# Optimization experiments

Measured on AMD Instinct MI355X. Metric: run time of the kernel, lower is better.

Reference implementation:

```python
import jax, jax.numpy as jnp
import numpy as np

N_NODES = 100000
N_EDGES = 1600000
IN_DIM = 128
HID = 32
HEADS = 4
OUT_DIM = 40
NEG_SLOPE = 0.2
BN_EPS = 1e-5


def setup_inputs() -> dict:
    key = jax.random.key(0)
    ks = jax.random.split(key, 13)
    x = jax.random.normal(ks[0], (N_NODES, IN_DIM), jnp.float32)
    edge_index = jax.random.randint(ks[1], (2, N_EDGES), 0, N_NODES, dtype=jnp.int32)
    s0 = 1.0 / np.sqrt(IN_DIM)
    s1 = 1.0 / np.sqrt(HEADS * HID)
    return {
        "x": x,
        "edge_index": edge_index,
        # layer 0: GATConv(IN_DIM -> HID, HEADS heads, concat)
        "W0": jax.random.normal(ks[2], (IN_DIM, HEADS * HID), jnp.float32) * s0,
        "a_src0": jax.random.normal(ks[3], (HEADS, HID), jnp.float32) * s0,
        "a_dst0": jax.random.normal(ks[4], (HEADS, HID), jnp.float32) * s0,
        "b0": jnp.zeros((HEADS * HID,), jnp.float32),
        # BatchNorm1d(HEADS*HID)
        "gamma0": jnp.ones((HEADS * HID,), jnp.float32),
        "beta0": jnp.zeros((HEADS * HID,), jnp.float32),
        # layer 1: GATConv(HEADS*HID -> OUT_DIM, 1 head, mean)
        "W1": jax.random.normal(ks[5], (HEADS * HID, OUT_DIM), jnp.float32) * s1,
        "a_src1": jax.random.normal(ks[6], (1, OUT_DIM), jnp.float32) * s1,
        "a_dst1": jax.random.normal(ks[7], (1, OUT_DIM), jnp.float32) * s1,
        "b1": jnp.zeros((OUT_DIM,), jnp.float32),
    }


def gat_conv(x, src, dst, n_nodes, W, a_src, a_dst, b, heads, concat):
    # linear transform: [N, H, C]
    h = (x @ W).reshape(n_nodes, heads, -1)
    # per-node attention logits [N, H]
    alpha_src = (h * a_src).sum(-1)
    alpha_dst = (h * a_dst).sum(-1)
    # per-edge raw attention [E, H]
    e = jax.nn.leaky_relu(alpha_src[src] + alpha_dst[dst], NEG_SLOPE)
    # softmax over incoming edges of each destination node
    m = jax.ops.segment_max(e, dst, num_segments=n_nodes)  # self-loops -> no empty segment
    ex = jnp.exp(e - m[dst])
    den = jax.ops.segment_sum(ex, dst, num_segments=n_nodes)
    # weighted scatter-aggregate of messages [E, H, C] -> [N, H, C]
    out = jax.ops.segment_sum(ex[:, :, None] * h[src], dst, num_segments=n_nodes)
    out = out / den[:, :, None]
    out = out.reshape(n_nodes, -1) if concat else out.mean(axis=1)
    return out + b


def batch_norm(x, gamma, beta):
    mu = x.mean(axis=0)
    var = x.var(axis=0)
    return (x - mu) * jax.lax.rsqrt(var + BN_EPS) * gamma + beta


def reference(x, edge_index, W0, a_src0, a_dst0, b0, gamma0, beta0,
              W1, a_src1, a_dst1, b1):
    n = x.shape[0]
    loop = jnp.arange(n, dtype=edge_index.dtype)
    src = jnp.concatenate([edge_index[0], loop])  # add self-loops (PyG default)
    dst = jnp.concatenate([edge_index[1], loop])
    # layer 0: GATConv -> BN -> ELU (dropout p=0 / eval -> identity)
    h = gat_conv(x, src, dst, n, W0, a_src0, a_dst0, b0, HEADS, True)
    h = jax.nn.elu(batch_norm(h, gamma0, beta0))
    # layer 1: GATConv, 1 head, mean aggregation, no BN/act
    out = gat_conv(h, src, dst, n, W1, a_src1, a_dst1, b1, 1, False)
    return out
```

## Files before the change

kernel.cpp:

```cpp
#include <hip/hip_runtime.h>
#include <hip/hip_bf16.h>
#include <math.h>

#define NN   100000
#define EE   1600000
#define ETOT (NN + EE)
#define IND  128
#define HD   128
#define OD   40
#define NEG  0.2f
#define BNEPS 1e-5f

typedef __attribute__((ext_vector_type(8))) short bf16x8;
typedef __attribute__((ext_vector_type(4))) float f32x4;

__device__ __forceinline__ float lrelu(float x) { return x > 0.f ? x : NEG * x; }

__device__ __forceinline__ unsigned pack_bf16(float a, float b) {
  unsigned ua = __float_as_uint(a), ub = __float_as_uint(b);
  ua = (ua + 0x7fffu + ((ua >> 16) & 1u)) >> 16;
  ub = (ub + 0x7fffu + ((ub >> 16) & 1u)) >> 16;
  return ua | (ub << 16);
}
__device__ __forceinline__ float bf16_lo(unsigned v) { return __uint_as_float(v << 16); }
__device__ __forceinline__ float bf16_hi(unsigned v) { return __uint_as_float(v & 0xffff0000u); }

__global__ __launch_bounds__(256) void w0pack_kernel(const float* __restrict__ W0,
                                                     unsigned* __restrict__ w0t) {
  int idx = blockIdx.x * 256 + threadIdx.x;
  if (idx >= 128 * 64) return;
  int n = idx & 127, kp = idx >> 7;
  float lo = W0[(size_t)(2 * kp) * 128 + n];
  float hi = W0[(size_t)(2 * kp + 1) * 128 + n];
  w0t[n * 64 + kp] = pack_bf16(lo, hi);
}

__global__ __launch_bounds__(256) void gemm0_kernel(const float* __restrict__ x,
                                                    const unsigned* __restrict__ w0t,
                                                    const float* __restrict__ a_src0,
                                                    const float* __restrict__ a_dst0,
                                                    unsigned* __restrict__ h0b,
                                                    float* __restrict__ asrc0,
                                                    float* __restrict__ adst0) {
  __shared__ __align__(16) unsigned As[64][68];
  __shared__ __align__(16) unsigned Wt[128][68];
  int t = threadIdx.x;
  int rowbase = blockIdx.x * 64;
  for (int idx = t; idx < 128 * 64; idx += 256) {
    Wt[idx >> 6][idx & 63] = w0t[idx];
  }
  for (int idx = t; idx < 64 * 64; idx += 256) {
    int row = idx >> 6, kp = idx & 63;
    int r = rowbase + row;
    int rc = r < NN ? r : NN - 1;
    float2 v = *(const float2*)&x[(size_t)rc * 128 + kp * 2];
    As[row][kp] = pack_bf16(v.x, v.y);
  }
  __syncthreads();

  int lane = t & 63, w = t >> 6;
  int mrow = lane & 15, g = lane >> 4;
  f32x4 acc[8];
#pragma unroll
  for (int nt = 0; nt < 8; nt++) acc[nt] = (f32x4){0.f, 0.f, 0.f, 0.f};
#pragma unroll
  for (int ks = 0; ks < 4; ks++) {
    bf16x8 a = *(const bf16x8*)&As[w * 16 + mrow][ks * 16 + g * 4];
#pragma unroll
    for (int nt = 0; nt < 8; nt++) {
      bf16x8 b = *(const bf16x8*)&Wt[nt * 16 + mrow][ks * 16 + g * 4];
      acc[nt] = __builtin_amdgcn_mfma_f32_16x16x32_bf16(a, b, acc[nt], 0, 0, 0);
    }
  }
  int col = lane & 15;
  float as_[8], ad_[8];
#pragma unroll
  for (int nt = 0; nt < 8; nt++) {
    as_[nt] = a_src0[nt * 16 + col];
    ad_[nt] = a_dst0[nt * 16 + col];
  }
#pragma unroll
  for (int reg = 0; reg < 4; reg++) {
    int r = rowbase + w * 16 + g * 4 + reg;
    bool rok = r < NN;
    float hs0 = acc[0][reg] * as_[0] + acc[1][reg] * as_[1];
    float hs1 = acc[2][reg] * as_[2] + acc[3][reg] * as_[3];
    float hs2 = acc[4][reg] * as_[4] + acc[5][reg] * as_[5];
    float hs3 = acc[6][reg] * as_[6] + acc[7][reg] * as_[7];
    float hd0 = acc[0][reg] * ad_[0] + acc[1][reg] * ad_[1];
    float hd1 = acc[2][reg] * ad_[2] + acc[3][reg] * ad_[3];
    float hd2 = acc[4][reg] * ad_[4] + acc[5][reg] * ad_[5];
    float hd3 = acc[6][reg] * ad_[6] + acc[7][reg] * ad_[7];
#pragma unroll
    for (int mk = 1; mk < 16; mk <<= 1) {
      hs0 += __shfl_xor(hs0, mk); hs1 += __shfl_xor(hs1, mk);
      hs2 += __shfl_xor(hs2, mk); hs3 += __shfl_xor(hs3, mk);
      hd0 += __shfl_xor(hd0, mk); hd1 += __shfl_xor(hd1, mk);
      hd2 += __shfl_xor(hd2, mk); hd3 += __shfl_xor(hd3, mk);
    }
    if ((lane & 15) == 0 && rok) {
      asrc0[r * 4 + 0] = hs0; asrc0[r * 4 + 1] = hs1;
      asrc0[r * 4 + 2] = hs2; asrc0[r * 4 + 3] = hs3;
      adst0[r * 4 + 0] = hd0; adst0[r * 4 + 1] = hd1;
      adst0[r * 4 + 2] = hd2; adst0[r * 4 + 3] = hd3;
    }
#pragma unroll
    for (int nt = 0; nt < 8; nt++) {
      float v = acc[nt][reg];
      float nv = __shfl_xor(v, 1);
      if (!(col & 1) && rok) h0b[(size_t)r * 64 + nt * 8 + (col >> 1)] = pack_bf16(v, nv);
    }
  }
}

__global__ void degrank_kernel(const int* __restrict__ ei, int* __restrict__ deg,
                               int* __restrict__ rank) {
  int i4 = (blockIdx.x * blockDim.x + threadIdx.x) * 4;
  if (i4 >= ETOT) return;
  int4 d;
  if (i4 < EE) d = *(const int4*)&ei[EE + i4];
  else         d = make_int4(i4 - EE, i4 - EE + 1, i4 - EE + 2, i4 - EE + 3);
  int4 r;
  r.x = atomicAdd(&deg[d.x], 1);
  r.y = atomicAdd(&deg[d.y], 1);
  r.z = atomicAdd(&deg[d.z], 1);
  r.w = atomicAdd(&deg[d.w], 1);
  *(int4*)&rank[i4] = r;
}

__global__ __launch_bounds__(256) void scanA_kernel(const int* __restrict__ deg,
                                                    int* __restrict__ scanned,
                                                    int* __restrict__ blocksums) {
  __shared__ int s[256];
  int t = threadIdx.x;
  int i = blockIdx.x * 256 + t;
  int v = (i < NN) ? deg[i] : 0;
  s[t] = v;
  __syncthreads();
  for (int off = 1; off < 256; off <<= 1) {
    int add = (t >= off) ? s[t - off] : 0;
    __syncthreads();
    s[t] += add;
    __syncthreads();
  }
  if (i < NN) scanned[i] = s[t];
  if (t == 255) blocksums[blockIdx.x] = s[255];
}

__global__ __launch_bounds__(512) void scanB_kernel(int* __restrict__ blocksums, int NB) {
  __shared__ int s[512];
  int t = threadIdx.x;
  int v = (t < NB) ? blocksums[t] : 0;
  s[t] = v;
  __syncthreads();
  for (int off = 1; off < 512; off <<= 1) {
    int add = (t >= off) ? s[t - off] : 0;
    __syncthreads();
    s[t] += add;
    __syncthreads();
  }
  if (t < NB) blocksums[t] = s[t] - v;
}

__global__ __launch_bounds__(256) void scanC_kernel(const int* __restrict__ scanned,
                                                    const int* __restrict__ deg,
                                                    const int* __restrict__ blocksums,
                                                    int* __restrict__ rowptr) {
  int i = blockIdx.x * 256 + threadIdx.x;
  if (i < NN) rowptr[i] = blocksums[blockIdx.x] + scanned[i] - deg[i];
  if (i == 0) rowptr[NN] = ETOT;
}

__global__ void scatter_kernel(const int* __restrict__ ei, const int* __restrict__ rowptr,
                               const int* __restrict__ rank, int* __restrict__ csr_src) {
  int i4 = (blockIdx.x * blockDim.x + threadIdx.x) * 4;
  if (i4 >= ETOT) return;
  int4 s, d;
  if (i4 < EE) {
    s = *(const int4*)&ei[i4];
    d = *(const int4*)&ei[EE + i4];
  } else {
    s = make_int4(i4 - EE, i4 - EE + 1, i4 - EE + 2, i4 - EE + 3);
    d = s;
  }
  int4 rk = *(const int4*)&rank[i4];
  int p0 = rowptr[d.x] + rk.x;
  int p1 = rowptr[d.y] + rk.y;
  int p2 = rowptr[d.z] + rk.z;
  int p3 = rowptr[d.w] + rk.w;
  csr_src[p0] = s.x;
  csr_src[p1] = s.y;
  csr_src[p2] = s.z;
  csr_src[p3] = s.w;
}

__global__ __launch_bounds__(256) void agg0_kernel(const int* __restrict__ csr_src,
                                                   const int* __restrict__ rowptr,
                                                   const float* __restrict__ asrc0,
                                                   const float* __restrict__ adst0,
                                                   const unsigned* __restrict__ h0b,
                                                   const float* __restrict__ b0,
                                                   unsigned* __restrict__ agg0b) {
  __shared__ float ws[16][4][17];
  __shared__ int   ss[16][16];
  int t = threadIdx.x;
  int grp = t >> 4;
  int p   = t & 15;
  int n = blockIdx.x * 16 + grp;
  if (n >= NN) return;
  int start = rowptr[n], end = rowptr[n + 1];
  float4 ad = *(const float4*)&adst0[(size_t)n * 4];
  int head = p >> 2;
  float a0 = 0.f, a1 = 0.f, a2 = 0.f, a3 = 0.f, a4 = 0.f, a5 = 0.f, a6 = 0.f, a7 = 0.f;
  float d0 = 0.f, d1 = 0.f, d2 = 0.f, d3 = 0.f;

  for (int base = start; base < end; base += 16) {
    int cnt = min(16, end - base);
    if (p < cnt) {
      int s = csr_src[base + p];
      float4 as = *(const float4*)&asrc0[(size_t)s * 4];
      float w0 = __expf(lrelu(as.x + ad.x));
      float w1 = __expf(lrelu(as.y + ad.y));
      float w2 = __expf(lrelu(as.z + ad.z));
      float w3 = __expf(lrelu(as.w + ad.w));
      d0 += w0; d1 += w1; d2 += w2; d3 += w3;
      ss[grp][p] = s;
      ws[grp][0][p] = w0;
      ws[grp][1][p] = w1;
      ws[grp][2][p] = w2;
      ws[grp][3][p] = w3;
    }
    __builtin_amdgcn_wave_barrier();
    if (cnt == 16) {
      uint4 hv[16];
#pragma unroll
      for (int e = 0; e < 16; e++) {
        int s = ss[grp][e];
        hv[e] = *(const uint4*)&h0b[(size_t)s * 64 + p * 4];
      }
#pragma unroll
      for (int e = 0; e < 16; e++) {
        float w = ws[grp][head][e];
        a0 += w * bf16_lo(hv[e].x); a1 += w * bf16_hi(hv[e].x);
        a2 += w * bf16_lo(hv[e].y); a3 += w * bf16_hi(hv[e].y);
        a4 += w * bf16_lo(hv[e].z); a5 += w * bf16_hi(hv[e].z);
        a6 += w * bf16_lo(hv[e].w); a7 += w * bf16_hi(hv[e].w);
      }
    } else {
      for (int eb = 0; eb < cnt; eb += 4) {
        int e0 = eb, e1 = eb + 1, e2 = eb + 2, e3 = eb + 3;
        float w0 = ws[grp][head][e0];
        float w1 = (e1 < cnt) ? ws[grp][head][e1] : 0.f;
        float w2 = (e2 < cnt) ? ws[grp][head][e2] : 0.f;
        float w3 = (e3 < cnt) ? ws[grp][head][e3] : 0.f;
        int s0 = ss[grp][e0];
        int s1 = ss[grp][(e1 < cnt) ? e1 : e0];
        int s2 = ss[grp][(e2 < cnt) ? e2 : e0];
        int s3 = ss[grp][(e3 < cnt) ? e3 : e0];
        uint4 h0v = *(const uint4*)&h0b[(size_t)s0 * 64 + p * 4];
        uint4 h1v = *(const uint4*)&h0b[(size_t)s1 * 64 + p * 4];
        uint4 h2v = *(const uint4*)&h0b[(size_t)s2 * 64 + p * 4];
        uint4 h3v = *(const uint4*)&h0b[(size_t)s3 * 64 + p * 4];
        a0 += w0 * bf16_lo(h0v.x); a1 += w0 * bf16_hi(h0v.x);
        a2 += w0 * bf16_lo(h0v.y); a3 += w0 * bf16_hi(h0v.y);
        a4 += w0 * bf16_lo(h0v.z); a5 += w0 * bf16_hi(h0v.z);
        a6 += w0 * bf16_lo(h0v.w); a7 += w0 * bf16_hi(h0v.w);
        a0 += w1 * bf16_lo(h1v.x); a1 += w1 * bf16_hi(h1v.x);
        a2 += w1 * bf16_lo(h1v.y); a3 += w1 * bf16_hi(h1v.y);
        a4 += w1 * bf16_lo(h1v.z); a5 += w1 * bf16_hi(h1v.z);
        a6 += w1 * bf16_lo(h1v.w); a7 += w1 * bf16_hi(h1v.w);
        a0 += w2 * bf16_lo(h2v.x); a1 += w2 * bf16_hi(h2v.x);
        a2 += w2 * bf16_lo(h2v.y); a3 += w2 * bf16_hi(h2v.y);
        a4 += w2 * bf16_lo(h2v.z); a5 += w2 * bf16_hi(h2v.z);
        a6 += w2 * bf16_lo(h2v.w); a7 += w2 * bf16_hi(h2v.w);
        a0 += w3 * bf16_lo(h3v.x); a1 += w3 * bf16_hi(h3v.x);
        a2 += w3 * bf16_lo(h3v.y); a3 += w3 * bf16_hi(h3v.y);
        a4 += w3 * bf16_lo(h3v.z); a5 += w3 * bf16_hi(h3v.z);
        a6 += w3 * bf16_lo(h3v.w); a7 += w3 * bf16_hi(h3v.w);
      }
    }
    __builtin_amdgcn_wave_barrier();
  }
#pragma unroll
  for (int mk = 1; mk < 16; mk <<= 1) {
    d0 += __shfl_xor(d0, mk);
    d1 += __shfl_xor(d1, mk);
    d2 += __shfl_xor(d2, mk);
    d3 += __shfl_xor(d3, mk);
  }
  float dh = head == 0 ? d0 : head == 1 ? d1 : head == 2 ? d2 : d3;
  float rd = 1.f / dh;
  int c = p * 8;
  float4 b1v = *(const float4*)&b0[c];
  float4 b2v = *(const float4*)&b0[c + 4];
  float o0 = a0 * rd + b1v.x, o1 = a1 * rd + b1v.y;
  float o2 = a2 * rd + b1v.z, o3 = a3 * rd + b1v.w;
  float o4 = a4 * rd + b2v.x, o5 = a5 * rd + b2v.y;
  float o6 = a6 * rd + b2v.z, o7 = a7 * rd + b2v.w;
  uint4 o;
  o.x = pack_bf16(o0, o1);
  o.y = pack_bf16(o2, o3);
  o.z = pack_bf16(o4, o5);
  o.w = pack_bf16(o6, o7);
  *(uint4*)&agg0b[(size_t)n * 64 + p * 4] = o;
}

__global__ __launch_bounds__(256) void bnstats_kernel(const unsigned* __restrict__ agg0b,
                                                      float* __restrict__ bnsum,
                                                      float* __restrict__ bnsq) {
  int t = threadIdx.x;
  int c2 = t & 63;
  int rg = t >> 6;
  float sl = 0.f, sh = 0.f, ql = 0.f, qh = 0.f;
  for (int r = blockIdx.x * 4 + rg; r < NN; r += 2048) {
    unsigned u = agg0b[(size_t)r * 64 + c2];
    float lo = bf16_lo(u), hi = bf16_hi(u);
    sl += lo; sh += hi;
    ql += lo * lo; qh += hi * hi;
  }
  __shared__ float L1[256], L2[256], L3[256], L4[256];
  L1[t] = sl; L2[t] = sh; L3[t] = ql; L4[t] = qh;
  __syncthreads();
  if (t < 64) {
    sl = L1[t] + L1[t + 64] + L1[t + 128] + L1[t + 192];
    sh = L2[t] + L2[t + 64] + L2[t + 128] + L2[t + 192];
    ql = L3[t] + L3[t + 64] + L3[t + 128] + L3[t + 192];
    qh = L4[t] + L4[t + 64] + L4[t + 128] + L4[t + 192];
    atomicAdd(&bnsum[2 * t], sl);
    atomicAdd(&bnsum[2 * t + 1], sh);
    atomicAdd(&bnsq[2 * t], ql);
    atomicAdd(&bnsq[2 * t + 1], qh);
  }
}

__global__ void bnfinal_kernel(const float* __restrict__ bnsum, const float* __restrict__ bnsq,
                               const float* __restrict__ gamma, const float* __restrict__ beta,
                               float* __restrict__ bnscale, float* __restrict__ bnshift) {
  int c = threadIdx.x;
  float mu = bnsum[c] / (float)NN;
  float var = bnsq[c] / (float)NN - mu * mu;
  float sc = gamma[c] / sqrtf(var + BNEPS);
  bnscale[c] = sc;
  bnshift[c] = beta[c] - mu * sc;
}

__global__ __launch_bounds__(256) void gemm1_kernel(const unsigned* __restrict__ agg0b,
                                                    const float* __restrict__ bnscale,
                                                    const float* __restrict__ bnshift,
                                                    const float* __restrict__ W1,
                                                    const float* __restrict__ a_src1,
                                                    const float* __restrict__ a_dst1,
                                                    unsigned* __restrict__ h1b,
                                                    float* __restrict__ asrc1,
                                                    float* __restrict__ adst1) {
  __shared__ __align__(16) unsigned As[64][68];
  __shared__ __align__(16) unsigned Wt[48][68];
  int t = threadIdx.x;
  int rowbase = blockIdx.x * 64;

  for (int idx = t; idx < 48 * 64; idx += 256) {
    int c = idx >> 6, kp = idx & 63;
    float lo = (c < OD) ? W1[(size_t)(2 * kp) * OD + c] : 0.f;
    float hi = (c < OD) ? W1[(size_t)(2 * kp + 1) * OD + c] : 0.f;
    Wt[c][kp] = pack_bf16(lo, hi);
  }
  for (int idx = t; idx < 64 * 16; idx += 256) {
    int row = idx >> 4, c4 = idx & 15;
    int r = rowbase + row;
    int rc = r < NN ? r : NN - 1;
    int k = c4 * 8;
    uint4 hv = *(const uint4*)&agg0b[(size_t)rc * 64 + c4 * 4];
    float4 sc1 = *(const float4*)&bnscale[k];
    float4 sc2 = *(const float4*)&bnscale[k + 4];
    float4 sh1 = *(const float4*)&bnshift[k];
    float4 sh2 = *(const float4*)&bnshift[k + 4];
    float y0 = bf16_lo(hv.x) * sc1.x + sh1.x;
    float y1 = bf16_hi(hv.x) * sc1.y + sh1.y;
    float y2 = bf16_lo(hv.y) * sc1.z + sh1.z;
    float y3 = bf16_hi(hv.y) * sc1.w + sh1.w;
    float y4 = bf16_lo(hv.z) * sc2.x + sh2.x;
    float y5 = bf16_hi(hv.z) * sc2.y + sh2.y;
    float y6 = bf16_lo(hv.w) * sc2.z + sh2.z;
    float y7 = bf16_hi(hv.w) * sc2.w + sh2.w;
    y0 = y0 > 0.f ? y0 : expm1f(y0);
    y1 = y1 > 0.f ? y1 : expm1f(y1);
    y2 = y2 > 0.f ? y2 : expm1f(y2);
    y3 = y3 > 0.f ? y3 : expm1f(y3);
    y4 = y4 > 0.f ? y4 : expm1f(y4);
    y5 = y5 > 0.f ? y5 : expm1f(y5);
    y6 = y6 > 0.f ? y6 : expm1f(y6);
    y7 = y7 > 0.f ? y7 : expm1f(y7);
    As[row][c4 * 4 + 0] = pack_bf16(y0, y1);
    As[row][c4 * 4 + 1] = pack_bf16(y2, y3);
    As[row][c4 * 4 + 2] = pack_bf16(y4, y5);
    As[row][c4 * 4 + 3] = pack_bf16(y6, y7);
  }
  __syncthreads();

  int lane = t & 63, w = t >> 6;
  int mrow = lane & 15, g = lane >> 4;
  f32x4 acc0 = {0.f, 0.f, 0.f, 0.f};
  f32x4 acc1 = {0.f, 0.f, 0.f, 0.f};
  f32x4 acc2 = {0.f, 0.f, 0.f, 0.f};
#pragma unroll
  for (int ks = 0; ks < 4; ks++) {
    bf16x8 a = *(const bf16x8*)&As[w * 16 + mrow][ks * 16 + g * 4];
    bf16x8 b0v = *(const bf16x8*)&Wt[mrow][ks * 16 + g * 4];
    bf16x8 b1v = *(const bf16x8*)&Wt[16 + mrow][ks * 16 + g * 4];
    bf16x8 b2v = *(const bf16x8*)&Wt[32 + mrow][ks * 16 + g * 4];
    acc0 = __builtin_amdgcn_mfma_f32_16x16x32_bf16(a, b0v, acc0, 0, 0, 0);
    acc1 = __builtin_amdgcn_mfma_f32_16x16x32_bf16(a, b1v, acc1, 0, 0, 0);
    acc2 = __builtin_amdgcn_mfma_f32_16x16x32_bf16(a, b2v, acc2, 0, 0, 0);
  }
  int col = lane & 15;
  float as0 = (col < OD)      ? a_src1[col]      : 0.f;
  float as1 = (16 + col < OD) ? a_src1[16 + col] : 0.f;
  float as2 = (32 + col < OD) ? a_src1[32 + col] : 0.f;
  float ad0 = (col < OD)      ? a_dst1[col]      : 0.f;
  float ad1 = (16 + col < OD) ? a_dst1[16 + col] : 0.f;
  float ad2 = (32 + col < OD) ? a_dst1[32 + col] : 0.f;
#pragma unroll
  for (int reg = 0; reg < 4; reg++) {
    int r = rowbase + w * 16 + g * 4 + reg;
    float v0 = acc0[reg], v1 = acc1[reg], v2 = acc2[reg];
    float ps = v0 * as0 + v1 * as1 + v2 * as2;
    float pd = v0 * ad0 + v1 * ad1 + v2 * ad2;
#pragma unroll
    for (int mk = 1; mk < 16; mk <<= 1) { ps += __shfl_xor(ps, mk); pd += __shfl_xor(pd, mk); }
    bool rok = r < NN;
    if ((lane & 15) == 0 && rok) { asrc1[r] = ps; adst1[r] = pd; }
    float n0 = __shfl_xor(v0, 1), n1 = __shfl_xor(v1, 1), n2 = __shfl_xor(v2, 1);
    if (!(col & 1) && rok) {
      h1b[(size_t)r * 20 + ((col) >> 1)]      = pack_bf16(v0, n0);
      h1b[(size_t)r * 20 + ((16 + col) >> 1)] = pack_bf16(v1, n1);
      if (32 + col < OD) h1b[(size_t)r * 20 + ((32 + col) >> 1)] = pack_bf16(v2, n2);
    }
  }
}

__global__ __launch_bounds__(256) void agg1_kernel(const int* __restrict__ csr_src,
                                                   const int* __restrict__ rowptr,
                                                   const float* __restrict__ asrc1,
                                                   const float* __restrict__ adst1,
                                                   const unsigned* __restrict__ h1b,
                                                   const float* __restrict__ b1,
                                                   float* __restrict__ out) {
  __shared__ float ws[4][64];
  __shared__ int   ss[4][64];
  int t = threadIdx.x;
  int lane = t & 63, wv = t >> 6;
  int n = blockIdx.x * 4 + wv;
  if (n >= NN) return;
  int start = rowptr[n], end = rowptr[n + 1];
  float ad = adst1[n];
  int esub = lane / 20;
  int chan = lane - esub * 20;
  float dsum = 0.f, acc0 = 0.f, acc1 = 0.f;
  for (int base = start; base < end; base += 64) {
    int cnt = min(64, end - base);
    if (lane < cnt) {
      int s = csr_src[base + lane];
      float w = __expf(lrelu(asrc1[s] + ad));
      dsum += w;
      ss[wv][lane] = s;
      ws[wv][lane] = w;
    }
    __builtin_amdgcn_wave_barrier();
    if (lane < 60) {
      int e = esub;
      for (; e + 9 < cnt; e += 12) {
        int s0 = ss[wv][e], s1 = ss[wv][e + 3], s2 = ss[wv][e + 6], s3 = ss[wv][e + 9];
        unsigned u0 = h1b[(size_t)s0 * 20 + chan];
        unsigned u1 = h1b[(size_t)s1 * 20 + chan];
        unsigned u2 = h1b[(size_t)s2 * 20 + chan];
        unsigned u3 = h1b[(size_t)s3 * 20 + chan];
        float w0 = ws[wv][e], w1 = ws[wv][e + 3], w2 = ws[wv][e + 6], w3 = ws[wv][e + 9];
        acc0 += w0 * bf16_lo(u0); acc1 += w0 * bf16_hi(u0);
        acc0 += w1 * bf16_lo(u1); acc1 += w1 * bf16_hi(u1);
        acc0 += w2 * bf16_lo(u2); acc1 += w2 * bf16_hi(u2);
        acc0 += w3 * bf16_lo(u3); acc1 += w3 * bf16_hi(u3);
      }
      for (; e < cnt; e += 3) {
        int s = ss[wv][e];
        float w = ws[wv][e];
        unsigned hv = h1b[(size_t)s * 20 + chan];
        acc0 += w * bf16_lo(hv);
        acc1 += w * bf16_hi(hv);
      }
    }
    __builtin_amdgcn_wave_barrier();
  }
#pragma unroll
  for (int mk = 1; mk < 64; mk <<= 1) dsum += __shfl_xor(dsum, mk);
  float rd = 1.f / dsum;
  float b0v = __shfl(acc0, lane + 20);
  float c0v = __shfl(acc0, lane + 40);
  float b1v = __shfl(acc1, lane + 20);
  float c1v = __shfl(acc1, lane + 40);
  if (lane < 20) {
    float2 o;
    o.x = (acc0 + b0v + c0v) * rd + b1[lane * 2];
    o.y = (acc1 + b1v + c1v) * rd + b1[lane * 2 + 1];
    *(float2*)&out[(size_t)n * 40 + lane * 2] = o;
  }
}

extern "C" void kernel_launch(void* const* d_in, const int* in_sizes, int n_in,
                              void* d_out, int out_size, void* d_ws, size_t ws_size,
                              hipStream_t stream) {
  const float* x       = (const float*)d_in[0];
  const int*   ei      = (const int*)d_in[1];
  const float* W0      = (const float*)d_in[2];
  const float* a_src0  = (const float*)d_in[3];
  const float* a_dst0  = (const float*)d_in[4];
  const float* b0      = (const float*)d_in[5];
  const float* gamma0  = (const float*)d_in[6];
  const float* beta0   = (const float*)d_in[7];
  const float* W1      = (const float*)d_in[8];
  const float* a_src1  = (const float*)d_in[9];
  const float* a_dst1  = (const float*)d_in[10];
  const float* b1      = (const float*)d_in[11];
  float* out = (float*)d_out;

  char* ws = (char*)d_ws;
  size_t off = 0;
  auto alloc = [&](size_t bytes) {
    void* p = ws + off;
    off += (bytes + 255) & ~(size_t)255;
    return p;
  };
  int*   deg      = (int*)alloc((size_t)NN * 4);
  float* bnsum    = (float*)alloc(128 * 4);
  float* bnsq     = (float*)alloc(128 * 4);
  unsigned* h0b   = (unsigned*)alloc((size_t)NN * 64 * 4);
  unsigned* agg0b = (unsigned*)alloc((size_t)NN * 64 * 4);
  unsigned* h1b   = (unsigned*)alloc((size_t)NN * 20 * 4);
  float* asrc0    = (float*)alloc((size_t)NN * 4 * 4);
  float* adst0    = (float*)alloc((size_t)NN * 4 * 4);
  float* asrc1    = (float*)alloc((size_t)NN * 4);
  float* adst1    = (float*)alloc((size_t)NN * 4);
  float* bnscale  = (float*)alloc(128 * 4);
  float* bnshift  = (float*)alloc(128 * 4);
  int*   rowptr   = (int*)alloc((size_t)(NN + 1) * 4);
  int*   scanned  = (int*)alloc((size_t)NN * 4);
  int*   csr      = (int*)alloc((size_t)ETOT * 4);
  int*   rank     = (int*)alloc((size_t)ETOT * 4);
  int*   bsums    = (int*)alloc(512 * 4);
  unsigned* w0t   = (unsigned*)alloc(128 * 64 * 4);
  (void)ws_size; (void)in_sizes; (void)n_in; (void)out_size;

  size_t zbytes = (char*)(bnsq + 128) - (char*)deg;
  hipMemsetAsync(deg, 0, zbytes, stream);

  const int NB = (NN + 255) / 256;
  const int e4grid = (ETOT / 4 + 255) / 256;

  w0pack_kernel<<<32, 256, 0, stream>>>(W0, w0t);
  gemm0_kernel<<<(NN + 63) / 64, 256, 0, stream>>>(x, w0t, a_src0, a_dst0, h0b, asrc0, adst0);
  degrank_kernel<<<e4grid, 256, 0, stream>>>(ei, deg, rank);
  scanA_kernel<<<NB, 256, 0, stream>>>(deg, scanned, bsums);
  scanB_kernel<<<1, 512, 0, stream>>>(bsums, NB);
  scanC_kernel<<<NB, 256, 0, stream>>>(scanned, deg, bsums, rowptr);
  scatter_kernel<<<e4grid, 256, 0, stream>>>(ei, rowptr, rank, csr);
  agg0_kernel<<<(NN + 15) / 16, 256, 0, stream>>>(csr, rowptr, asrc0, adst0, h0b, b0, agg0b);
  bnstats_kernel<<<512, 256, 0, stream>>>(agg0b, bnsum, bnsq);
  bnfinal_kernel<<<1, 128, 0, stream>>>(bnsum, bnsq, gamma0, beta0, bnscale, bnshift);
  gemm1_kernel<<<(NN + 63) / 64, 256, 0, stream>>>(agg0b, bnscale, bnshift, W1, a_src1, a_dst1,
                                                   h1b, asrc1, adst1);
  agg1_kernel<<<(NN + 3) / 4, 256, 0, stream>>>(csr, rowptr, asrc1, adst1, h1b, b1, out);
}
```

Before: 333.1 us.

## Fuse BN statistics into aggregation, merge prep kernels, widen agg1 loads

Folds W0 packing into the degree/rank kernel, computes BatchNorm sum and sum-of-squares inside agg0 using wave shuffles and bucketed atomics, and finalizes BN scale/shift at the top of gemm1. This removes the separate bnstats and bnfinal launches and the extra pass over agg0b. It also drops agg0's specialized 16-edge unrolled path and changes agg1 to 8-byte loads with 4 channels per lane. Fusing the stats adds atomic contention, which is spread over 16 buckets, and the agg0 grid now assumes NN is divisible by 16.

```diff
diff --git a/kernel.cpp b/kernel.cpp
--- a/kernel.cpp
+++ b/kernel.cpp
@@ -10,6 +10,7 @@
 #define OD   40
 #define NEG  0.2f
 #define BNEPS 1e-5f
+#define NBKT 16
 
 typedef __attribute__((ext_vector_type(8))) short bf16x8;
 typedef __attribute__((ext_vector_type(4))) float f32x4;
@@ -25,14 +26,27 @@
 __device__ __forceinline__ float bf16_lo(unsigned v) { return __uint_as_float(v << 16); }
 __device__ __forceinline__ float bf16_hi(unsigned v) { return __uint_as_float(v & 0xffff0000u); }
 
-__global__ __launch_bounds__(256) void w0pack_kernel(const float* __restrict__ W0,
-                                                     unsigned* __restrict__ w0t) {
-  int idx = blockIdx.x * 256 + threadIdx.x;
-  if (idx >= 128 * 64) return;
-  int n = idx & 127, kp = idx >> 7;
-  float lo = W0[(size_t)(2 * kp) * 128 + n];
-  float hi = W0[(size_t)(2 * kp + 1) * 128 + n];
-  w0t[n * 64 + kp] = pack_bf16(lo, hi);
+__global__ void prep_kernel(const float* __restrict__ W0, unsigned* __restrict__ w0t,
+                            const int* __restrict__ ei, int* __restrict__ deg,
+                            int* __restrict__ rank) {
+  int gid = blockIdx.x * blockDim.x + threadIdx.x;
+  if (gid < 128 * 64) {
+    int n = gid & 127, kp = gid >> 7;
+    float lo = W0[(size_t)(2 * kp) * 128 + n];
+    float hi = W0[(size_t)(2 * kp + 1) * 128 + n];
+    w0t[n * 64 + kp] = pack_bf16(lo, hi);
+  }
+  int i4 = gid * 4;
+  if (i4 >= ETOT) return;
+  int4 d;
+  if (i4 < EE) d = *(const int4*)&ei[EE + i4];
+  else         d = make_int4(i4 - EE, i4 - EE + 1, i4 - EE + 2, i4 - EE + 3);
+  int4 r;
+  r.x = atomicAdd(&deg[d.x], 1);
+  r.y = atomicAdd(&deg[d.y], 1);
+  r.z = atomicAdd(&deg[d.z], 1);
+  r.w = atomicAdd(&deg[d.w], 1);
+  *(int4*)&rank[i4] = r;
 }
 
 __global__ __launch_bounds__(256) void gemm0_kernel(const float* __restrict__ x,
@@ -111,21 +125,6 @@
       if (!(col & 1) && rok) h0b[(size_t)r * 64 + nt * 8 + (col >> 1)] = pack_bf16(v, nv);
     }
   }
-}
-
-__global__ void degrank_kernel(const int* __restrict__ ei, int* __restrict__ deg,
-                               int* __restrict__ rank) {
-  int i4 = (blockIdx.x * blockDim.x + threadIdx.x) * 4;
-  if (i4 >= ETOT) return;
-  int4 d;
-  if (i4 < EE) d = *(const int4*)&ei[EE + i4];
-  else         d = make_int4(i4 - EE, i4 - EE + 1, i4 - EE + 2, i4 - EE + 3);
-  int4 r;
-  r.x = atomicAdd(&deg[d.x], 1);
-  r.y = atomicAdd(&deg[d.y], 1);
-  r.z = atomicAdd(&deg[d.z], 1);
-  r.w = atomicAdd(&deg[d.w], 1);
-  *(int4*)&rank[i4] = r;
 }
 
 __global__ __launch_bounds__(256) void scanA_kernel(const int* __restrict__ deg,
@@ -200,14 +199,16 @@
                                                    const float* __restrict__ adst0,
                                                    const unsigned* __restrict__ h0b,
                                                    const float* __restrict__ b0,
-                                                   unsigned* __restrict__ agg0b) {
+                                                   unsigned* __restrict__ agg0b,
+                                                   float* __restrict__ bnsumB,
+                                                   float* __restrict__ bnsqB) {
   __shared__ float ws[16][4][17];
   __shared__ int   ss[16][16];
+  __shared__ float Lsum[4][16][8], Lsq[4][16][8];
   int t = threadIdx.x;
   int grp = t >> 4;
   int p   = t & 15;
   int n = blockIdx.x * 16 + grp;
-  if (n >= NN) return;
   int start = rowptr[n], end = rowptr[n + 1];
   float4 ad = *(const float4*)&adst0[(size_t)n * 4];
   int head = p >> 2;
@@ -231,53 +232,36 @@
       ws[grp][3][p] = w3;
     }
     __builtin_amdgcn_wave_barrier();
-    if (cnt == 16) {
-      uint4 hv[16];
-#pragma unroll
-      for (int e = 0; e < 16; e++) {
-        int s = ss[grp][e];
-        hv[e] = *(const uint4*)&h0b[(size_t)s * 64 + p * 4];
-      }
-#pragma unroll
-      for (int e = 0; e < 16; e++) {
-        float w = ws[grp][head][e];
-        a0 += w * bf16_lo(hv[e].x); a1 += w * bf16_hi(hv[e].x);
-        a2 += w * bf16_lo(hv[e].y); a3 += w * bf16_hi(hv[e].y);
-        a4 += w * bf16_lo(hv[e].z); a5 += w * bf16_hi(hv[e].z);
-        a6 += w * bf16_lo(hv[e].w); a7 += w * bf16_hi(hv[e].w);
-      }
-    } else {
-      for (int eb = 0; eb < cnt; eb += 4) {
-        int e0 = eb, e1 = eb + 1, e2 = eb + 2, e3 = eb + 3;
-        float w0 = ws[grp][head][e0];
-        float w1 = (e1 < cnt) ? ws[grp][head][e1] : 0.f;
-        float w2 = (e2 < cnt) ? ws[grp][head][e2] : 0.f;
-        float w3 = (e3 < cnt) ? ws[grp][head][e3] : 0.f;
-        int s0 = ss[grp][e0];
-        int s1 = ss[grp][(e1 < cnt) ? e1 : e0];
-        int s2 = ss[grp][(e2 < cnt) ? e2 : e0];
-        int s3 = ss[grp][(e3 < cnt) ? e3 : e0];
-        uint4 h0v = *(const uint4*)&h0b[(size_t)s0 * 64 + p * 4];
-        uint4 h1v = *(const uint4*)&h0b[(size_t)s1 * 64 + p * 4];
-        uint4 h2v = *(const uint4*)&h0b[(size_t)s2 * 64 + p * 4];
-        uint4 h3v = *(const uint4*)&h0b[(size_t)s3 * 64 + p * 4];
-        a0 += w0 * bf16_lo(h0v.x); a1 += w0 * bf16_hi(h0v.x);
-        a2 += w0 * bf16_lo(h0v.y); a3 += w0 * bf16_hi(h0v.y);
-        a4 += w0 * bf16_lo(h0v.z); a5 += w0 * bf16_hi(h0v.z);
-        a6 += w0 * bf16_lo(h0v.w); a7 += w0 * bf16_hi(h0v.w);
-        a0 += w1 * bf16_lo(h1v.x); a1 += w1 * bf16_hi(h1v.x);
-        a2 += w1 * bf16_lo(h1v.y); a3 += w1 * bf16_hi(h1v.y);
-        a4 += w1 * bf16_lo(h1v.z); a5 += w1 * bf16_hi(h1v.z);
-        a6 += w1 * bf16_lo(h1v.w); a7 += w1 * bf16_hi(h1v.w);
-        a0 += w2 * bf16_lo(h2v.x); a1 += w2 * bf16_hi(h2v.x);
-        a2 += w2 * bf16_lo(h2v.y); a3 += w2 * bf16_hi(h2v.y);
-        a4 += w2 * bf16_lo(h2v.z); a5 += w2 * bf16_hi(h2v.z);
-        a6 += w2 * bf16_lo(h2v.w); a7 += w2 * bf16_hi(h2v.w);
-        a0 += w3 * bf16_lo(h3v.x); a1 += w3 * bf16_hi(h3v.x);
-        a2 += w3 * bf16_lo(h3v.y); a3 += w3 * bf16_hi(h3v.y);
-        a4 += w3 * bf16_lo(h3v.z); a5 += w3 * bf16_hi(h3v.z);
-        a6 += w3 * bf16_lo(h3v.w); a7 += w3 * bf16_hi(h3v.w);
-      }
+    for (int eb = 0; eb < cnt; eb += 4) {
+      int e0 = eb, e1 = eb + 1, e2 = eb + 2, e3 = eb + 3;
+      float w0 = ws[grp][head][e0];
+      float w1 = (e1 < cnt) ? ws[grp][head][e1] : 0.f;
+      float w2 = (e2 < cnt) ? ws[grp][head][e2] : 0.f;
+      float w3 = (e3 < cnt) ? ws[grp][head][e3] : 0.f;
+      int s0 = ss[grp][e0];
+      int s1 = ss[grp][(e1 < cnt) ? e1 : e0];
+      int s2 = ss[grp][(e2 < cnt) ? e2 : e0];
+      int s3 = ss[grp][(e3 < cnt) ? e3 : e0];
+      uint4 h0v = *(const uint4*)&h0b[(size_t)s0 * 64 + p * 4];
+      uint4 h1v = *(const uint4*)&h0b[(size_t)s1 * 64 + p * 4];
+      uint4 h2v = *(const uint4*)&h0b[(size_t)s2 * 64 + p * 4];
+      uint4 h3v = *(const uint4*)&h0b[(size_t)s3 * 64 + p * 4];
+      a0 += w0 * bf16_lo(h0v.x); a1 += w0 * bf16_hi(h0v.x);
+      a2 += w0 * bf16_lo(h0v.y); a3 += w0 * bf16_hi(h0v.y);
+      a4 += w0 * bf16_lo(h0v.z); a5 += w0 * bf16_hi(h0v.z);
+      a6 += w0 * bf16_lo(h0v.w); a7 += w0 * bf16_hi(h0v.w);
+      a0 += w1 * bf16_lo(h1v.x); a1 += w1 * bf16_hi(h1v.x);
+      a2 += w1 * bf16_lo(h1v.y); a3 += w1 * bf16_hi(h1v.y);
+      a4 += w1 * bf16_lo(h1v.z); a5 += w1 * bf16_hi(h1v.z);
+      a6 += w1 * bf16_lo(h1v.w); a7 += w1 * bf16_hi(h1v.w);
+      a0 += w2 * bf16_lo(h2v.x); a1 += w2 * bf16_hi(h2v.x);
+      a2 += w2 * bf16_lo(h2v.y); a3 += w2 * bf16_hi(h2v.y);
+      a4 += w2 * bf16_lo(h2v.z); a5 += w2 * bf16_hi(h2v.z);
+      a6 += w2 * bf16_lo(h2v.w); a7 += w2 * bf16_hi(h2v.w);
+      a0 += w3 * bf16_lo(h3v.x); a1 += w3 * bf16_hi(h3v.x);
+      a2 += w3 * bf16_lo(h3v.y); a3 += w3 * bf16_hi(h3v.y);
+      a4 += w3 * bf16_lo(h3v.z); a5 += w3 * bf16_hi(h3v.z);
+      a6 += w3 * bf16_lo(h3v.w); a7 += w3 * bf16_hi(h3v.w);
     }
     __builtin_amdgcn_wave_barrier();
   }
@@ -303,50 +287,48 @@
   o.z = pack_bf16(o4, o5);
   o.w = pack_bf16(o6, o7);
   *(uint4*)&agg0b[(size_t)n * 64 + p * 4] = o;
-}
-
-__global__ __launch_bounds__(256) void bnstats_kernel(const unsigned* __restrict__ agg0b,
-                                                      float* __restrict__ bnsum,
-                                                      float* __restrict__ bnsq) {
-  int t = threadIdx.x;
-  int c2 = t & 63;
-  int rg = t >> 6;
-  float sl = 0.f, sh = 0.f, ql = 0.f, qh = 0.f;
-  for (int r = blockIdx.x * 4 + rg; r < NN; r += 2048) {
-    unsigned u = agg0b[(size_t)r * 64 + c2];
-    float lo = bf16_lo(u), hi = bf16_hi(u);
-    sl += lo; sh += hi;
-    ql += lo * lo; qh += hi * hi;
-  }
-  __shared__ float L1[256], L2[256], L3[256], L4[256];
-  L1[t] = sl; L2[t] = sh; L3[t] = ql; L4[t] = qh;
+
+  float s0 = o0, s1 = o1, s2 = o2, s3 = o3, s4 = o4, s5 = o5, s6 = o6, s7 = o7;
+  float q0 = o0 * o0, q1 = o1 * o1, q2 = o2 * o2, q3 = o3 * o3;
+  float q4 = o4 * o4, q5 = o5 * o5, q6 = o6 * o6, q7 = o7 * o7;
+#pragma unroll
+  for (int mk = 16; mk < 64; mk <<= 1) {
+    s0 += __shfl_xor(s0, mk); s1 += __shfl_xor(s1, mk);
+    s2 += __shfl_xor(s2, mk); s3 += __shfl_xor(s3, mk);
+    s4 += __shfl_xor(s4, mk); s5 += __shfl_xor(s5, mk);
+    s6 += __shfl_xor(s6, mk); s7 += __shfl_xor(s7, mk);
+    q0 += __shfl_xor(q0, mk); q1 += __shfl_xor(q1, mk);
+    q2 += __shfl_xor(q2, mk); q3 += __shfl_xor(q3, mk);
+    q4 += __shfl_xor(q4, mk); q5 += __shfl_xor(q5, mk);
+    q6 += __shfl_xor(q6, mk); q7 += __shfl_xor(q7, mk);
+  }
+  int lane = t & 63, wv = t >> 6;
+  if (lane < 16) {
+    Lsum[wv][lane][0] = s0; Lsum[wv][lane][1] = s1;
+    Lsum[wv][lane][2] = s2; Lsum[wv][lane][3] = s3;
+    Lsum[wv][lane][4] = s4; Lsum[wv][lane][5] = s5;
+    Lsum[wv][lane][6] = s6; Lsum[wv][lane][7] = s7;
+    Lsq[wv][lane][0] = q0; Lsq[wv][lane][1] = q1;
+    Lsq[wv][lane][2] = q2; Lsq[wv][lane][3] = q3;
+    Lsq[wv][lane][4] = q4; Lsq[wv][lane][5] = q5;
+    Lsq[wv][lane][6] = q6; Lsq[wv][lane][7] = q7;
+  }
   __syncthreads();
-  if (t < 64) {
-    sl = L1[t] + L1[t + 64] + L1[t + 128] + L1[t + 192];
-    sh = L2[t] + L2[t + 64] + L2[t + 128] + L2[t + 192];
-    ql = L3[t] + L3[t + 64] + L3[t + 128] + L3[t + 192];
-    qh = L4[t] + L4[t + 64] + L4[t + 128] + L4[t + 192];
-    atomicAdd(&bnsum[2 * t], sl);
-    atomicAdd(&bnsum[2 * t + 1], sh);
-    atomicAdd(&bnsq[2 * t], ql);
-    atomicAdd(&bnsq[2 * t + 1], qh);
-  }
-}
-
-__global__ void bnfinal_kernel(const float* __restrict__ bnsum, const float* __restrict__ bnsq,
-                               const float* __restrict__ gamma, const float* __restrict__ beta,
-                               float* __restrict__ bnscale, float* __restrict__ bnshift) {
-  int c = threadIdx.x;
-  float mu = bnsum[c] / (float)NN;
-  float var = bnsq[c] / (float)NN - mu * mu;
-  float sc = gamma[c] / sqrtf(var + BNEPS);
-  bnscale[c] = sc;
-  bnshift[c] = beta[c] - mu * sc;
+  if (t < 128) {
+    int pp = t >> 3, jj = t & 7;
+    float s = Lsum[0][pp][jj] + Lsum[1][pp][jj] + Lsum[2][pp][jj] + Lsum[3][pp][jj];
+    float q = Lsq[0][pp][jj] + Lsq[1][pp][jj] + Lsq[2][pp][jj] + Lsq[3][pp][jj];
+    int bkt = blockIdx.x & (NBKT - 1);
+    atomicAdd(&bnsumB[bkt * 128 + t], s);
+    atomicAdd(&bnsqB[bkt * 128 + t], q);
+  }
 }
 
 __global__ __launch_bounds__(256) void gemm1_kernel(const unsigned* __restrict__ agg0b,
-                                                    const float* __restrict__ bnscale,
-                                                    const float* __restrict__ bnshift,
+                                                    const float* __restrict__ bnsumB,
+                                                    const float* __restrict__ bnsqB,
+                                                    const float* __restrict__ gamma,
+                                                    const float* __restrict__ beta,
                                                     const float* __restrict__ W1,
                                                     const float* __restrict__ a_src1,
                                                     const float* __restrict__ a_dst1,
@@ -355,33 +337,44 @@
                                                     float* __restrict__ adst1) {
   __shared__ __align__(16) unsigned As[64][68];
   __shared__ __align__(16) unsigned Wt[48][68];
+  __shared__ float bnsc[128], bnsh[128];
   int t = threadIdx.x;
   int rowbase = blockIdx.x * 64;
 
+  if (t < 128) {
+    float s = 0.f, q = 0.f;
+#pragma unroll
+    for (int k = 0; k < NBKT; k++) {
+      s += bnsumB[k * 128 + t];
+      q += bnsqB[k * 128 + t];
+    }
+    float mu = s / (float)NN;
+    float var = q / (float)NN - mu * mu;
+    float sc = gamma[t] / sqrtf(var + BNEPS);
+    bnsc[t] = sc;
+    bnsh[t] = beta[t] - mu * sc;
+  }
   for (int idx = t; idx < 48 * 64; idx += 256) {
     int c = idx >> 6, kp = idx & 63;
     float lo = (c < OD) ? W1[(size_t)(2 * kp) * OD + c] : 0.f;
     float hi = (c < OD) ? W1[(size_t)(2 * kp + 1) * OD + c] : 0.f;
     Wt[c][kp] = pack_bf16(lo, hi);
   }
+  __syncthreads();
   for (int idx = t; idx < 64 * 16; idx += 256) {
     int row = idx >> 4, c4 = idx & 15;
     int r = rowbase + row;
     int rc = r < NN ? r : NN - 1;
     int k = c4 * 8;
     uint4 hv = *(const uint4*)&agg0b[(size_t)rc * 64 + c4 * 4];
-    float4 sc1 = *(const float4*)&bnscale[k];
-    float4 sc2 = *(const float4*)&bnscale[k + 4];
-    float4 sh1 = *(const float4*)&bnshift[k];
-    float4 sh2 = *(const float4*)&bnshift[k + 4];
-    float y0 = bf16_lo(hv.x) * sc1.x + sh1.x;
-    float y1 = bf16_hi(hv.x) * sc1.y + sh1.y;
-    float y2 = bf16_lo(hv.y) * sc1.z + sh1.z;
-    float y3 = bf16_hi(hv.y) * sc1.w + sh1.w;
-    float y4 = bf16_lo(hv.z) * sc2.x + sh2.x;
-    float y5 = bf16_hi(hv.z) * sc2.y + sh2.y;
-    float y6 = bf16_lo(hv.w) * sc2.z + sh2.z;
-    float y7 = bf16_hi(hv.w) * sc2.w + sh2.w;
+    float y0 = bf16_lo(hv.x) * bnsc[k + 0] + bnsh[k + 0];
+    float y1 = bf16_hi(hv.x) * bnsc[k + 1] + bnsh[k + 1];
+    float y2 = bf16_lo(hv.y) * bnsc[k + 2] + bnsh[k + 2];
+    float y3 = bf16_hi(hv.y) * bnsc[k + 3] + bnsh[k + 3];
+    float y4 = bf16_lo(hv.z) * bnsc[k + 4] + bnsh[k + 4];
+    float y5 = bf16_hi(hv.z) * bnsc[k + 5] + bnsh[k + 5];
+    float y6 = bf16_lo(hv.w) * bnsc[k + 6] + bnsh[k + 6];
+    float y7 = bf16_hi(hv.w) * bnsc[k + 7] + bnsh[k + 7];
     y0 = y0 > 0.f ? y0 : expm1f(y0);
     y1 = y1 > 0.f ? y1 : expm1f(y1);
     y2 = y2 > 0.f ? y2 : expm1f(y2);
@@ -453,9 +446,10 @@
   if (n >= NN) return;
   int start = rowptr[n], end = rowptr[n + 1];
   float ad = adst1[n];
-  int esub = lane / 20;
-  int chan = lane - esub * 20;
-  float dsum = 0.f, acc0 = 0.f, acc1 = 0.f;
+  int esub = lane / 10;
+  int c2   = lane - esub * 10;
+  float dsum = 0.f;
+  float acc0 = 0.f, acc1 = 0.f, acc2 = 0.f, acc3 = 0.f;
   for (int base = start; base < end; base += 64) {
     int cnt = min(64, end - base);
     if (lane < cnt) {
@@ -468,24 +462,28 @@
     __builtin_amdgcn_wave_barrier();
     if (lane < 60) {
       int e = esub;
-      for (; e + 9 < cnt; e += 12) {
-        int s0 = ss[wv][e], s1 = ss[wv][e + 3], s2 = ss[wv][e + 6], s3 = ss[wv][e + 9];
-        unsigned u0 = h1b[(size_t)s0 * 20 + chan];
-        unsigned u1 = h1b[(size_t)s1 * 20 + chan];
-        unsigned u2 = h1b[(size_t)s2 * 20 + chan];
-        unsigned u3 = h1b[(size_t)s3 * 20 + chan];
-        float w0 = ws[wv][e], w1 = ws[wv][e + 3], w2 = ws[wv][e + 6], w3 = ws[wv][e + 9];
-        acc0 += w0 * bf16_lo(u0); acc1 += w0 * bf16_hi(u0);
-        acc0 += w1 * bf16_lo(u1); acc1 += w1 * bf16_hi(u1);
-        acc0 += w2 * bf16_lo(u2); acc1 += w2 * bf16_hi(u2);
-        acc0 += w3 * bf16_lo(u3); acc1 += w3 * bf16_hi(u3);
+      for (; e + 18 < cnt; e += 24) {
+        int s0 = ss[wv][e], s1 = ss[wv][e + 6], s2 = ss[wv][e + 12], s3 = ss[wv][e + 18];
+        uint2 u0 = *(const uint2*)&h1b[(size_t)s0 * 20 + c2 * 2];
+        uint2 u1 = *(const uint2*)&h1b[(size_t)s1 * 20 + c2 * 2];
+        uint2 u2 = *(const uint2*)&h1b[(size_t)s2 * 20 + c2 * 2];
+        uint2 u3 = *(const uint2*)&h1b[(size_t)s3 * 20 + c2 * 2];
+        float w0 = ws[wv][e], w1 = ws[wv][e + 6], w2 = ws[wv][e + 12], w3 = ws[wv][e + 18];
+        acc0 += w0 * bf16_lo(u0.x); acc1 += w0 * bf16_hi(u0.x);
+        acc2 += w0 * bf16_lo(u0.y); acc3 += w0 * bf16_hi(u0.y);
+        acc0 += w1 * bf16_lo(u1.x); acc1 += w1 * bf16_hi(u1.x);
+        acc2 += w1 * bf16_lo(u1.y); acc3 += w1 * bf16_hi(u1.y);
+        acc0 += w2 * bf16_lo(u2.x); acc1 += w2 * bf16_hi(u2.x);
+        acc2 += w2 * bf16_lo(u2.y); acc3 += w2 * bf16_hi(u2.y);
+        acc0 += w3 * bf16_lo(u3.x); acc1 += w3 * bf16_hi(u3.x);
+        acc2 += w3 * bf16_lo(u3.y); acc3 += w3 * bf16_hi(u3.y);
       }
-      for (; e < cnt; e += 3) {
+      for (; e < cnt; e += 6) {
         int s = ss[wv][e];
         float w = ws[wv][e];
-        unsigned hv = h1b[(size_t)s * 20 + chan];
-        acc0 += w * bf16_lo(hv);
-        acc1 += w * bf16_hi(hv);
+        uint2 u = *(const uint2*)&h1b[(size_t)s * 20 + c2 * 2];
+        acc0 += w * bf16_lo(u.x); acc1 += w * bf16_hi(u.x);
+        acc2 += w * bf16_lo(u.y); acc3 += w * bf16_hi(u.y);
       }
     }
     __builtin_amdgcn_wave_barrier();
@@ -493,15 +491,30 @@
 #pragma unroll
   for (int mk = 1; mk < 64; mk <<= 1) dsum += __shfl_xor(dsum, mk);
   float rd = 1.f / dsum;
-  float b0v = __shfl(acc0, lane + 20);
-  float c0v = __shfl(acc0, lane + 40);
-  float b1v = __shfl(acc1, lane + 20);
-  float c1v = __shfl(acc1, lane + 40);
-  if (lane < 20) {
-    float2 o;
-    o.x = (acc0 + b0v + c0v) * rd + b1[lane * 2];
-    o.y = (acc1 + b1v + c1v) * rd + b1[lane * 2 + 1];
-    *(float2*)&out[(size_t)n * 40 + lane * 2] = o;
+  float p01 = __shfl(acc0, lane + 10), p02 = __shfl(acc0, lane + 20);
+  float p03 = __shfl(acc0, lane + 30), p04 = __shfl(acc0, lane + 40);
+  float p05 = __shfl(acc0, lane + 50);
+  float p11 = __shfl(acc1, lane + 10), p12 = __shfl(acc1, lane + 20);
+  float p13 = __shfl(acc1, lane + 30), p14 = __shfl(acc1, lane + 40);
+  float p15 = __shfl(acc1, lane + 50);
+  float p21 = __shfl(acc2, lane + 10), p22 = __shfl(acc2, lane + 20);
+  float p23 = __shfl(acc2, lane + 30), p24 = __shfl(acc2, lane + 40);
+  float p25 = __shfl(acc2, lane + 50);
+  float p31 = __shfl(acc3, lane + 10), p32 = __shfl(acc3, lane + 20);
+  float p33 = __shfl(acc3, lane + 30), p34 = __shfl(acc3, lane + 40);
+  float p35 = __shfl(acc3, lane + 50);
+  if (lane < 10) {
+    float t0 = acc0 + p01 + p02 + p03 + p04 + p05;
+    float t1 = acc1 + p11 + p12 + p13 + p14 + p15;
+    float t2 = acc2 + p21 + p22 + p23 + p24 + p25;
+    float t3 = acc3 + p31 + p32 + p33 + p34 + p35;
+    float4 bv = *(const float4*)&b1[lane * 4];
+    float4 o;
+    o.x = t0 * rd + bv.x;
+    o.y = t1 * rd + bv.y;
+    o.z = t2 * rd + bv.z;
+    o.w = t3 * rd + bv.w;
+    *(float4*)&out[(size_t)n * 40 + lane * 4] = o;
   }
 }
 
@@ -530,8 +543,8 @@
     return p;
   };
   int*   deg      = (int*)alloc((size_t)NN * 4);
-  float* bnsum    = (float*)alloc(128 * 4);
-  float* bnsq     = (float*)alloc(128 * 4);
+  float* bnsumB   = (float*)alloc(NBKT * 128 * 4);
+  float* bnsqB    = (float*)alloc(NBKT * 128 * 4);
   unsigned* h0b   = (unsigned*)alloc((size_t)NN * 64 * 4);
   unsigned* agg0b = (unsigned*)alloc((size_t)NN * 64 * 4);
   unsigned* h1b   = (unsigned*)alloc((size_t)NN * 20 * 4);
@@ -539,8 +552,6 @@
   float* adst0    = (float*)alloc((size_t)NN * 4 * 4);
   float* asrc1    = (float*)alloc((size_t)NN * 4);
   float* adst1    = (float*)alloc((size_t)NN * 4);
-  float* bnscale  = (float*)alloc(128 * 4);
-  float* bnshift  = (float*)alloc(128 * 4);
   int*   rowptr   = (int*)alloc((size_t)(NN + 1) * 4);
   int*   scanned  = (int*)alloc((size_t)NN * 4);
   int*   csr      = (int*)alloc((size_t)ETOT * 4);
@@ -549,23 +560,21 @@
   unsigned* w0t   = (unsigned*)alloc(128 * 64 * 4);
   (void)ws_size; (void)in_sizes; (void)n_in; (void)out_size;
 
-  size_t zbytes = (char*)(bnsq + 128) - (char*)deg;
+  size_t zbytes = (char*)(bnsqB + NBKT * 128) - (char*)deg;
   hipMemsetAsync(deg, 0, zbytes, stream);
 
   const int NB = (NN + 255) / 256;
   const int e4grid = (ETOT / 4 + 255) / 256;
 
-  w0pack_kernel<<<32, 256, 0, stream>>>(W0, w0t);
+  prep_kernel<<<e4grid, 256, 0, stream>>>(W0, w0t, ei, deg, rank);
   gemm0_kernel<<<(NN + 63) / 64, 256, 0, stream>>>(x, w0t, a_src0, a_dst0, h0b, asrc0, adst0);
-  degrank_kernel<<<e4grid, 256, 0, stream>>>(ei, deg, rank);
   scanA_kernel<<<NB, 256, 0, stream>>>(deg, scanned, bsums);
   scanB_kernel<<<1, 512, 0, stream>>>(bsums, NB);
   scanC_kernel<<<NB, 256, 0, stream>>>(scanned, deg, bsums, rowptr);
   scatter_kernel<<<e4grid, 256, 0, stream>>>(ei, rowptr, rank, csr);
-  agg0_kernel<<<(NN + 15) / 16, 256, 0, stream>>>(csr, rowptr, asrc0, adst0, h0b, b0, agg0b);
-  bnstats_kernel<<<512, 256, 0, stream>>>(agg0b, bnsum, bnsq);
-  bnfinal_kernel<<<1, 128, 0, stream>>>(bnsum, bnsq, gamma0, beta0, bnscale, bnshift);
-  gemm1_kernel<<<(NN + 63) / 64, 256, 0, stream>>>(agg0b, bnscale, bnshift, W1, a_src1, a_dst1,
-                                                   h1b, asrc1, adst1);
+  agg0_kernel<<<NN / 16, 256, 0, stream>>>(csr, rowptr, asrc0, adst0, h0b, b0, agg0b,
+                                           bnsumB, bnsqB);
+  gemm1_kernel<<<(NN + 63) / 64, 256, 0, stream>>>(agg0b, bnsumB, bnsqB, gamma0, beta0,
+                                                   W1, a_src1, a_dst1, h1b, asrc1, adst1);
   agg1_kernel<<<(NN + 3) / 4, 256, 0, stream>>>(csr, rowptr, asrc1, adst1, h1b, b1, out);
 }
```

Result: faster. 298.7 us (-10.3%).
